# Performance work log

Measured on AMD Instinct MI355X. Metric: run time of the kernel, lower is better.

Reference implementation:

```python
import jax, jax.numpy as jnp
import numpy as np

D = 640          # feature dim (x_dim)
C = 64           # number of classes
N = 1024         # support samples (16 shots/class)
Q = 2048         # query samples
REG = 0.3        # reg_param


def setup_inputs() -> dict:
    key = jax.random.key(0)
    k0, k1, k2, k3, k4 = jax.random.split(key, 5)
    X = jax.random.normal(k0, (N, D), jnp.float32)
    y = (jnp.arange(N) % C).astype(jnp.int32)          # every class populated
    Xq = jax.random.normal(k1, (Q, D), jnp.float32)
    # learnable prior parameters (perturbed from the torch init so grads are nontrivial)
    m = 0.02 * jax.random.normal(k2, (1, D), jnp.float32)
    kappa = jnp.array([0.1], jnp.float32)
    nu = jnp.array([float(D)], jnp.float32)
    triu_diag = 1.0 + 0.05 * jax.random.normal(k3, (D,), jnp.float32)
    triu_lower = jnp.eye(D, dtype=jnp.float32) + 0.05 * jax.random.normal(k4, (D, D), jnp.float32)
    return {"X": X, "y": y, "Xq": Xq, "m": m, "kappa": kappa, "nu": nu,
            "triu_diag": triu_diag, "triu_lower": triu_lower}


def reference(X, y, Xq, m, kappa, nu, triu_diag, triu_lower):
    # strictly-lower-triangular mask: triu(ones, 1).T
    mask = jnp.triu(jnp.ones((D, D), X.dtype), 1).T
    L = jnp.diag(jnp.abs(triu_diag)) + triu_lower * mask          # Cholesky-like factor
    kappa_ = jnp.abs(kappa[0]) + 1e-6
    nu_ = jnp.maximum(nu[0], D - 1 + 1e-6)

    onehot = jax.nn.one_hot(y, C, dtype=X.dtype)                   # [N, C]
    Nc = onehot.sum(0)                                             # [C]
    mean_c = (onehot.T @ X) / Nc[:, None]                          # [C, D]
    # MAP posterior mean per class
    w = Nc / (kappa_ + Nc)
    mu = (1.0 - w)[:, None] * m + w[:, None] * mean_c              # [C, D]

    # per-class second moment: S_c = sum_{y=c} x x^T (segmented X^T X)
    Xc = onehot.T[:, :, None] * X[None, :, :]                      # [C, N, D]
    S = jnp.einsum('cnd,ne->cde', Xc, X)                           # [C, D, D]

    LLt = L @ L.T
    mm = m.T @ m                                                   # [D, D]
    mu_outer = jnp.einsum('cd,ce->cde', mu, mu)
    sigma = (LLt[None] + S + kappa_ * mm[None]
             - (kappa_ + Nc)[:, None, None] * mu_outer)
    sigma = sigma / (nu_ + Nc + D + 2)[:, None, None]
    sigma_inv = jnp.linalg.inv(sigma)
    sigma_inv = (1.0 - REG) * sigma_inv + REG * jnp.eye(D, dtype=X.dtype)

    # batched Mahalanobis quadratic form: -(x - mu_c)^T Sinv_c (x - mu_c)
    diff = Xq[:, None, :] - mu[None, :, :]                         # [Q, C, D]
    dist = jnp.einsum('qcd,cde,qce->qc', diff, sigma_inv, diff)
    return -dist
```

## Files before the change

kernel.cpp:

```cpp
#include <hip/hip_runtime.h>
#include <hip/hip_bf16.h>


#define D 640
#define C 64
#define NSUP 1024
#define Q 2048
#define KMAX 16
#define R18 18
#define VROWS (C * R18)
#define YROWS 3137
#define YPAD 3200
#define NEXT 704

typedef __attribute__((ext_vector_type(8))) short bf16x8;
typedef __attribute__((ext_vector_type(4))) float floatx4;

__device__ __forceinline__ unsigned short f2bf(float x) {
    unsigned int u = __float_as_uint(x);
    unsigned int r = u + 0x7FFFu + ((u >> 16) & 1u);
    return (unsigned short)(r >> 16);
}

__global__ void k_setup(const int* __restrict__ y, const float* __restrict__ kappa,
                        const float* __restrict__ nu, const float* __restrict__ diag,
                        int* __restrict__ cnt, int* __restrict__ idx,
                        float* __restrict__ sc, float* __restrict__ rd,
                        int* __restrict__ rowmap) {
    __shared__ int lc[C];
    int tid = threadIdx.x;
    if (tid < C) lc[tid] = 0;
    __syncthreads();
    for (int n = tid; n < NSUP; n += 256) {
        int c = y[n];
        int k = atomicAdd(&lc[c], 1);
        if (k < KMAX) idx[c * KMAX + k] = n;
    }
    __syncthreads();
    for (int d = tid; d < D; d += 256) rd[d] = 1.0f / fabsf(diag[d]);
    if (tid < C) {
        int n = lc[tid]; if (n > KMAX) n = KMAX;
        cnt[tid] = n;
        float kap = fabsf(kappa[0]) + 1e-6f;
        float nuv = fmaxf(nu[0], (float)(D - 1) + 1e-6f);
        float Ncf = (float)n;
        sc[64 + tid]  = Ncf / (kap + Ncf);
        sc[128 + tid] = nuv + Ncf + (float)(D + 2);
        sc[192 + tid] = -1.0f / (kap + Ncf);
        if (tid == 0) { sc[0] = kap; sc[1] = nuv; }
    }
    __syncthreads();
    for (int i = tid; i < VROWS; i += 256) {
        int c = i / R18, j = i - c * R18;
        int nc = lc[c] < KMAX ? lc[c] : KMAX;
        int rm;
        if (j == 0) rm = Q + NSUP;
        else if (j <= KMAX) rm = (j - 1 < nc) ? Q + idx[c * KMAX + j - 1] : -1;
        else rm = Q + NSUP + 1 + c;
        rowmap[i] = rm;
    }
}

__global__ __launch_bounds__(256) void k_dinv_mu(
        const float* __restrict__ tlow, const float* __restrict__ rd,
        float* __restrict__ Linv,
        const float* __restrict__ X, const float* __restrict__ m,
        const int* __restrict__ cnt, const int* __restrict__ idx,
        const float* __restrict__ sc, float* __restrict__ mu) {
    __shared__ float Lst[128 * 128];
    int tid = threadIdx.x;
    if (blockIdx.x < 160) {
        int bid = blockIdx.x;
        int b = bid >> 5;
        int j = ((bid & 31) << 2) + (tid >> 6);
        int lane = tid & 63;
        int bB = b * 128;
        {
            float4 tv[16];
            float rv[16];
#pragma unroll
            for (int u = 0; u < 16; ++u) {
                int e = tid + u * 256;
                int c4 = (e & 31) * 4, r = e >> 5;
                tv[u] = *(const float4*)(tlow + (size_t)(bB + r) * D + bB + c4);
                rv[u] = rd[bB + r];
            }
#pragma unroll
            for (int u = 0; u < 16; ++u) {
                int e = tid + u * 256;
                int c4 = (e & 31) * 4, r = e >> 5;
                float vv[4] = {tv[u].x, tv[u].y, tv[u].z, tv[u].w};
#pragma unroll
                for (int t = 0; t < 4; ++t) {
                    int c = c4 + t;
                    float v;
                    if (r == c) v = 1.0f;
                    else if (r > c) v = rv[u] * vv[t];
                    else v = 0.f;
                    Lst[c * 128 + (r ^ (c & 63))] = v;
                }
            }
        }
        __syncthreads();
        float rd0 = rd[bB + lane], rd1 = rd[bB + 64 + lane];
        float acc0 = 0.f, acc1 = 0.f, zz0 = 0.f, zz1 = 0.f;
        for (int i = j; i < 128; ++i) {
            int ri = i >> 6, il = i & 63;
            float av = (ri == 0) ? acc0 : acc1;
            float ai = __shfl(av, il);
            float zi = (i == j) ? __shfl((ri == 0) ? rd0 : rd1, il) : -ai;
            int sw = i & 63;
            float l0 = Lst[i * 128 + (lane ^ sw)];
            float l1 = Lst[i * 128 + 64 + (lane ^ sw)];
            if (lane > i) acc0 += l0 * zi;
            if (64 + lane > i) acc1 += l1 * zi;
            if (lane == i) zz0 = zi;
            if (64 + lane == i) zz1 = zi;
        }
        Linv[(size_t)(bB + lane) * D + bB + j] = zz0;
        Linv[(size_t)(bB + 64 + lane) * D + bB + j] = zz1;
    } else {
        int u = (blockIdx.x - 160) * 2 + (tid >> 7);
        int c = u / 5, by = u - c * 5;
        int d = by * 128 + (tid & 127);
        int n = cnt[c];
        float s = 0.f;
        for (int k = 0; k < n; ++k) s += X[(size_t)idx[c * KMAX + k] * D + d];
        float w = sc[64 + c];
        float mean = (n > 0) ? s / (float)n : 0.f;
        mu[(size_t)c * D + d] = (1.f - w) * m[d] + w * mean;
    }
}

__global__ void k_lhat(const float* __restrict__ tlow, const float* __restrict__ Linv,
                       float* __restrict__ Lhat) {
    const int bi_tab[10] = {1, 2, 2, 3, 3, 3, 4, 4, 4, 4};
    const int bk_tab[10] = {0, 0, 1, 0, 1, 2, 0, 1, 2, 3};
    int p = blockIdx.y;
    int bi = bi_tab[p], bk = bk_tab[p];
    int tid = threadIdx.x;
    int c = tid & 127;
    int r = (blockIdx.x << 1) + (tid >> 7);
    const float* drow = Linv + (size_t)(bi * 128 + r) * D + bi * 128;
    const float* lcol = tlow + (size_t)(bi * 128) * D + bk * 128 + c;
    float s = 0.f;
#pragma unroll 4
    for (int t = 0; t < 128; ++t) s += drow[t] * lcol[(size_t)t * D];
    Lhat[(size_t)(bi * 128 + r) * D + bk * 128 + c] = s;
}

template<int B>
__device__ __forceinline__ void linv_chain(const float* __restrict__ Lhat,
                                           float* __restrict__ Linv,
                                           float S[4][128][20],
                                           int cB, int tid) {
    const int ty = tid >> 2, tx = tid & 3;
    const int r0 = 2 * ty;
    float acc[4 - B][2][4];
#pragma unroll
    for (int a = 0; a < 4 - B; ++a)
#pragma unroll
        for (int rr = 0; rr < 2; ++rr)
#pragma unroll
            for (int cc = 0; cc < 4; ++cc) acc[a][rr][cc] = 0.f;
#pragma unroll
    for (int js = 0; js < 4 - B; ++js) {
        const int j = B + js;
        for (int k0 = 0; k0 < 128; k0 += 8) {
            float svf[8][4];
#pragma unroll
            for (int u = 0; u < 8; ++u) {
                float4 s4 = *(const float4*)&S[js][k0 + u][tx * 4];
                svf[u][0] = s4.x; svf[u][1] = s4.y; svf[u][2] = s4.z; svf[u][3] = s4.w;
            }
#pragma unroll
            for (int a = js; a < 4 - B; ++a) {
                const int i = B + 1 + a;
                const float* p0 = Lhat + (size_t)(i * 128 + r0) * D + j * 128 + k0;
                const float* p1 = p0 + D;
                float4 a00 = *(const float4*)(p0);
                float4 a01 = *(const float4*)(p0 + 4);
                float4 a10 = *(const float4*)(p1);
                float4 a11 = *(const float4*)(p1 + 4);
                float ar0[8] = {a00.x, a00.y, a00.z, a00.w, a01.x, a01.y, a01.z, a01.w};
                float ar1[8] = {a10.x, a10.y, a10.z, a10.w, a11.x, a11.y, a11.z, a11.w};
#pragma unroll
                for (int u = 0; u < 8; ++u) {
#pragma unroll
                    for (int cc = 0; cc < 4; ++cc) {
                        acc[a][0][cc] += ar0[u] * svf[u][cc];
                        acc[a][1][cc] += ar1[u] * svf[u][cc];
                    }
                }
            }
        }
        {
            const int i = j + 1;
#pragma unroll
            for (int rr = 0; rr < 2; ++rr) {
                const int r = r0 + rr;
                float4 v;
                v.x = -acc[js][rr][0]; v.y = -acc[js][rr][1];
                v.z = -acc[js][rr][2]; v.w = -acc[js][rr][3];
                if (js + 1 < 4 - B) *(float4*)&S[js + 1][r][tx * 4] = v;
                *(float4*)(Linv + (size_t)(i * 128 + r) * D + cB + tx * 4) = v;
            }
        }
        if (js + 1 < 4 - B) __syncthreads();
    }
}

__global__ __launch_bounds__(256) void k_linv_fill(const float* __restrict__ Lhat,
                                                   float* __restrict__ Linv) {
    __shared__ __align__(16) float S[4][128][20];
    int tid = threadIdx.x;
    int b = blockIdx.x >> 3, strip = blockIdx.x & 7;
    int bB = b * 128, cB = bB + strip * 16;
    {
        int r = tid >> 1, c0 = (tid & 1) * 8;
        const float* src = Linv + (size_t)(bB + r) * D + cB + c0;
        *(float4*)&S[0][r][c0]     = *(const float4*)(src);
        *(float4*)&S[0][r][c0 + 4] = *(const float4*)(src + 4);
    }
    __syncthreads();
    if (b == 0)      linv_chain<0>(Lhat, Linv, S, cB, tid);
    else if (b == 1) linv_chain<1>(Lhat, Linv, S, cB, tid);
    else if (b == 2) linv_chain<2>(Lhat, Linv, S, cB, tid);
    else             linv_chain<3>(Lhat, Linv, S, cB, tid);
}

__device__ __forceinline__ void pack4(const float* vv, unsigned short* hp, unsigned short* lp) {
#pragma unroll
    for (int i = 0; i < 4; ++i) {
        unsigned short hb = f2bf(vv[i]);
        float hf = __uint_as_float((unsigned int)hb << 16);
        hp[i] = hb;
        lp[i] = f2bf(vv[i] - hf);
    }
}

__device__ __forceinline__ void rownorm_body(const float* __restrict__ A, int ld,
                                             float* __restrict__ out, int gw, int lane) {
    const float* row = A + (size_t)gw * ld;
    float s = 0.f;
    for (int d = lane; d < D; d += 64) { float v = row[d]; s += v * v; }
#pragma unroll
    for (int off = 32; off; off >>= 1) s += __shfl_xor(s, off);
    if (lane == 0) out[gw] = s;
}

__global__ void k_packA(const float* __restrict__ Xq, const float* __restrict__ X,
                        const float* __restrict__ m, const float* __restrict__ mu,
                        unsigned short* __restrict__ Ah, unsigned short* __restrict__ Al,
                        const float* __restrict__ Linv,
                        unsigned short* __restrict__ Bh, unsigned short* __restrict__ Bl,
                        float* __restrict__ a0) {
    int bid = blockIdx.x, tid = threadIdx.x;
    if (bid < 2000) {
        int gid = bid * 256 + tid;
        int row = gid / 160, c = (gid - row * 160) * 4;
        if (row >= YPAD) return;
        float4 v = {0.f, 0.f, 0.f, 0.f};
        if (row < Q) v = *(const float4*)(Xq + (size_t)row * D + c);
        else if (row < Q + NSUP) v = *(const float4*)(X + (size_t)(row - Q) * D + c);
        else if (row == Q + NSUP) v = *(const float4*)(m + c);
        else if (row < YROWS) v = *(const float4*)(mu + (size_t)(row - (Q + NSUP + 1)) * D + c);
        float vv[4] = {v.x, v.y, v.z, v.w};
        ushort4 h, l;
        pack4(vv, (unsigned short*)&h, (unsigned short*)&l);
        *(ushort4*)(Ah + (size_t)row * D + c) = h;
        *(ushort4*)(Al + (size_t)row * D + c) = l;
    } else if (bid < 2440) {
        int gid = (bid - 2000) * 256 + tid;
        int row = gid / 160, c = (gid - row * 160) * 4;
        if (row >= NEXT) return;
        float4 v;
        if (row < D) v = *(const float4*)(Linv + (size_t)row * D + c);
        else v = *(const float4*)(mu + (size_t)(row - D) * D + c);
        float vv[4] = {v.x, v.y, v.z, v.w};
#pragma unroll
        for (int i = 0; i < 4; ++i)
            if (row < D && c + i > row) vv[i] = 0.f;
        ushort4 h, l;
        pack4(vv, (unsigned short*)&h, (unsigned short*)&l);
        *(ushort4*)(Bh + (size_t)row * D + c) = h;
        *(ushort4*)(Bl + (size_t)row * D + c) = l;
    } else {
        int gw = ((bid - 2440) * 256 + tid) >> 6;
        rownorm_body(Xq, D, a0, gw, tid & 63);
    }
}

__global__ __launch_bounds__(256) void k_mfma_nt(
        const unsigned short* __restrict__ Ah, const unsigned short* __restrict__ Al,
        const unsigned short* __restrict__ Bh, const unsigned short* __restrict__ Bl,
        const int* __restrict__ rowmap, float* __restrict__ Out,
        int M, int N, int ldo) {
    __shared__ unsigned short Ah_s[64 * 32], Al_s[64 * 32];
    __shared__ unsigned short Bh_s[64 * 32], Bl_s[64 * 32];
    int tid = threadIdx.x;
    int rowBase = blockIdx.y * 64, colBase = blockIdx.x * 64;
    int r = tid >> 2, e = (tid & 3) << 3;
    int gr = rowBase + r;
    int gc = colBase + r;
    int br = (gc < N) ? (rowmap ? rowmap[gc] : gc) : -1;
    bool aok = (gr < M);
    int w = tid >> 6, lane = tid & 63, q = lane >> 4, lr = lane & 15;
    int aoff = (16 * w + lr) * 32 + q * 8;
    const uint4 z4 = {0u, 0u, 0u, 0u};
    floatx4 acc[4] = {{0.f, 0.f, 0.f, 0.f}, {0.f, 0.f, 0.f, 0.f},
                      {0.f, 0.f, 0.f, 0.f}, {0.f, 0.f, 0.f, 0.f}};
    for (int kk = 0; kk < D; kk += 32) {
        uint4 vah = aok ? *(const uint4*)(Ah + (size_t)gr * D + kk + e) : z4;
        uint4 val = aok ? *(const uint4*)(Al + (size_t)gr * D + kk + e) : z4;
        uint4 vbh = (br >= 0) ? *(const uint4*)(Bh + (size_t)br * D + kk + e) : z4;
        uint4 vbl = (br >= 0) ? *(const uint4*)(Bl + (size_t)br * D + kk + e) : z4;
        __syncthreads();
        *(uint4*)(Ah_s + r * 32 + e) = vah;
        *(uint4*)(Al_s + r * 32 + e) = val;
        *(uint4*)(Bh_s + r * 32 + e) = vbh;
        *(uint4*)(Bl_s + r * 32 + e) = vbl;
        __syncthreads();
        bf16x8 ah = *(const bf16x8*)(Ah_s + aoff);
        bf16x8 al = *(const bf16x8*)(Al_s + aoff);
#pragma unroll
        for (int tt = 0; tt < 4; ++tt) {
            int boff = (16 * tt + lr) * 32 + q * 8;
            bf16x8 bh = *(const bf16x8*)(Bh_s + boff);
            bf16x8 bl = *(const bf16x8*)(Bl_s + boff);
            acc[tt] = __builtin_amdgcn_mfma_f32_16x16x32_bf16(ah, bh, acc[tt], 0, 0, 0);
            acc[tt] = __builtin_amdgcn_mfma_f32_16x16x32_bf16(ah, bl, acc[tt], 0, 0, 0);
            acc[tt] = __builtin_amdgcn_mfma_f32_16x16x32_bf16(al, bh, acc[tt], 0, 0, 0);
        }
    }
#pragma unroll
    for (int tt = 0; tt < 4; ++tt) {
        int gc2 = colBase + 16 * tt + lr;
#pragma unroll
        for (int rg = 0; rg < 4; ++rg) {
            int gr2 = rowBase + 16 * w + q * 4 + rg;
            if (gr2 < M && gc2 < N) Out[(size_t)gr2 * ldo + gc2] = acc[tt][rg];
        }
    }
}

__global__ __launch_bounds__(256) void k_packB(
        const float* __restrict__ Yt, const int* __restrict__ rowmap,
        const float* __restrict__ mu, const float* __restrict__ sc,
        unsigned short* __restrict__ Th, unsigned short* __restrict__ Tl,
        float* __restrict__ at,
        float* __restrict__ h, float* __restrict__ btil,
        float* __restrict__ b0, float* __restrict__ kinv) {
    __shared__ __align__(16) float sv[R18][644];
    __shared__ float aug[R18][40];
    __shared__ int rmv[R18];
    int tid = threadIdx.x;
    if (blockIdx.x < 64) {
        int c = blockIdx.x;
        if (tid < R18) rmv[tid] = rowmap[c * R18 + tid];
        __syncthreads();
        {
            int rmu[12];
#pragma unroll
            for (int u = 0; u < 12; ++u) {
                int i = tid + u * 256;
                int r = i / 160;
                rmu[u] = (i < R18 * 160) ? rmv[r] : -1;
            }
            float4 buf[12];
            const float4 z = {0.f, 0.f, 0.f, 0.f};
#pragma unroll
            for (int u = 0; u < 12; ++u) {
                int i = tid + u * 256;
                int d4 = (i - (i / 160) * 160) * 4;
                buf[u] = (rmu[u] >= 0) ? *(const float4*)(Yt + (size_t)rmu[u] * NEXT + d4) : z;
            }
#pragma unroll
            for (int u = 0; u < 12; ++u) {
                int i = tid + u * 256;
                if (i < R18 * 160) {
                    int r = i / 160, d4 = (i - r * 160) * 4;
                    *(float4*)&sv[r][d4] = buf[u];
                }
            }
        }
        __syncthreads();
        if (tid < 171) {
            int i = 0, rem = tid;
            while (rem >= R18 - i) { rem -= R18 - i; ++i; }
            int j = i + rem;
            const float* ri = sv[i];
            const float* rj = sv[j];
            float s0 = 0.f, s1 = 0.f, s2 = 0.f, s3 = 0.f;
#pragma unroll 4
            for (int d = 0; d < D; d += 4) {
                float4 a = *(const float4*)(ri + d);
                float4 bb = *(const float4*)(rj + d);
                s0 += a.x * bb.x; s1 += a.y * bb.y;
                s2 += a.z * bb.z; s3 += a.w * bb.w;
            }
            float s = (s0 + s1) + (s2 + s3);
            aug[i][j] = s;
            if (i != j) aug[j][i] = s;
        }
        for (int i2 = tid; i2 < R18 * R18; i2 += 256)
            aug[i2 / R18][R18 + i2 % R18] = (i2 / R18 == i2 % R18) ? 1.f : 0.f;
        __syncthreads();
        int w = tid >> 6, lane = tid & 63;
        if (w == 1) {
            const float* mc = mu + (size_t)c * D;
            float s = 0.f;
            for (int d = lane; d < D; d += 64) { float v = mc[d]; s += v * v; }
#pragma unroll
            for (int off = 32; off; off >>= 1) s += __shfl_xor(s, off);
            if (lane == 0) b0[c] = s;
        }
        if (w == 0) {
            if (lane < R18) h[c * R18 + lane] = aug[lane][R18 - 1];
            if (lane == 0) btil[c] = aug[R18 - 1][R18 - 1];
            volatile float (*va)[40] = (volatile float (*)[40])aug;
            if (lane == 0) va[0][0] += 1.0f / sc[0];
            else if (lane <= KMAX) va[lane][lane] += 1.0f;
            else if (lane == R18 - 1) va[R18 - 1][R18 - 1] += sc[192 + c];
            __threadfence_block();
            for (int p = 0; p < R18; ++p) {
                float v = (lane >= p && lane < R18) ? fabsf(va[lane][p]) : -1.f;
                int bi = lane;
#pragma unroll
                for (int off = 32; off; off >>= 1) {
                    float ov = __shfl_xor(v, off);
                    int oi = __shfl_xor(bi, off);
                    if (ov > v || (ov == v && oi < bi)) { v = ov; bi = oi; }
                }
                float pv = va[bi][p];
                if (lane < 2 * R18) {
                    float rp = va[bi][lane];
                    if (bi != p) va[bi][lane] = va[p][lane];
                    va[p][lane] = rp / pv;
                }
                __threadfence_block();
                float f  = (lane < R18) ? va[lane][p] : 0.f;
                float pr = (lane < 2 * R18) ? va[p][lane] : 0.f;
#pragma unroll
                for (int it = 0; it < 11; ++it) {
                    int e = lane + it * 64;
                    int r2 = e / 36, cc = e - r2 * 36;
                    float fr = __shfl(f, r2 < R18 ? r2 : 0);
                    float pc = __shfl(pr, cc);
                    if (e < R18 * 2 * R18 && r2 != p) va[r2][cc] -= fr * pc;
                }
                __threadfence_block();
            }
            for (int e = lane; e < R18 * R18; e += 64)
                kinv[(size_t)c * R18 * R18 + e] = va[e / R18][R18 + e % R18];
        }
    } else if (blockIdx.x < 2064) {
        int gid = (blockIdx.x - 64) * 256 + tid;
        int row = gid / 160, c = (gid - row * 160) * 4;
        if (row >= YPAD) return;
        float4 v = *(const float4*)(Yt + (size_t)row * NEXT + c);
        float vv[4] = {v.x, v.y, v.z, v.w};
        ushort4 hh, ll;
        pack4(vv, (unsigned short*)&hh, (unsigned short*)&ll);
        *(ushort4*)(Th + (size_t)row * D + c) = hh;
        *(ushort4*)(Tl + (size_t)row * D + c) = ll;
    } else {
        int gw = ((blockIdx.x - 2064) * 256 + tid) >> 6;
        rownorm_body(Yt, NEXT, at, gw, tid & 63);
    }
}

__global__ void k_epi(const float* __restrict__ G, const float* __restrict__ Yt,
                      const float* __restrict__ at, const float* __restrict__ a0,
                      const float* __restrict__ h, const float* __restrict__ btil,
                      const float* __restrict__ b0, const float* __restrict__ kinv,
                      const float* __restrict__ sc, float* __restrict__ out) {
    __shared__ float lk[R18 * R18], lh[R18];
    __shared__ float ldn, lbt, lb0;
    int c = blockIdx.x, tid = threadIdx.x;
    for (int i = tid; i < R18 * R18; i += 256) lk[i] = kinv[(size_t)c * R18 * R18 + i];
    if (tid < R18) lh[tid] = h[c * R18 + tid];
    if (tid == 0) { ldn = sc[128 + c]; lbt = btil[c]; lb0 = b0[c]; }
    __syncthreads();
    int q = blockIdx.y * 256 + tid;
    const float* Gr = G + (size_t)q * VROWS + c * R18;
    float g[R18];
#pragma unroll
    for (int j = 0; j < R18; ++j) g[j] = Gr[j];
    float ipt = g[R18 - 1];
#pragma unroll
    for (int j = 0; j < R18; ++j) g[j] -= lh[j];
    float corr = 0.f;
#pragma unroll
    for (int i = 0; i < R18; ++i) {
        float s = 0.f;
#pragma unroll
        for (int j = 0; j < R18; ++j) s += lk[i * R18 + j] * g[j];
        corr += g[i] * s;
    }
    float ip0 = Yt[(size_t)q * NEXT + D + c];
    float tt = at[q] - 2.f * ipt + lbt;
    float t0 = a0[q] - 2.f * ip0 + lb0;
    out[(size_t)q * C + c] = -(0.7f * ldn * (tt - corr) + 0.3f * t0);
}

extern "C" void kernel_launch(void* const* d_in, const int* in_sizes, int n_in,
                              void* d_out, int out_size, void* d_ws, size_t ws_size,
                              hipStream_t stream) {
    const float* X     = (const float*)d_in[0];
    const int*   y     = (const int*)d_in[1];
    const float* Xq    = (const float*)d_in[2];
    const float* m     = (const float*)d_in[3];
    const float* kappa = (const float*)d_in[4];
    const float* nu    = (const float*)d_in[5];
    const float* tdiag = (const float*)d_in[6];
    const float* tlow  = (const float*)d_in[7];
    float* out = (float*)d_out;

    char* w = (char*)d_ws;
    auto alloc = [&](size_t bytes) {
        char* p = w;
        w += (bytes + 255) & ~(size_t)255;
        return p;
    };
    int*   cnt    = (int*)alloc(C * 4);
    int*   idx    = (int*)alloc(C * KMAX * 4);
    int*   rowmap = (int*)alloc(VROWS * 4);
    float* sc     = (float*)alloc(256 * 4);
    float* rd     = (float*)alloc(D * 4);
    float* mu     = (float*)alloc((size_t)C * D * 4);
    float* at     = (float*)alloc(Q * 4);
    float* a0     = (float*)alloc(Q * 4);
    float* h      = (float*)alloc(C * R18 * 4);
    float* btil   = (float*)alloc(C * 4);
    float* b0     = (float*)alloc(C * 4);
    float* kinv   = (float*)alloc((size_t)C * R18 * R18 * 4);
    float* Ytout  = (float*)alloc((size_t)YPAD * NEXT * 4);
    unsigned short* Th = (unsigned short*)alloc((size_t)YPAD * D * 2);
    unsigned short* Tl = (unsigned short*)alloc((size_t)YPAD * D * 2);
    unsigned short* Bh = (unsigned short*)alloc((size_t)NEXT * D * 2);
    unsigned short* Bl = (unsigned short*)alloc((size_t)NEXT * D * 2);
    char* wmark = w;
    float* Linv = (float*)alloc((size_t)D * D * 4);
    float* Lhat = (float*)alloc((size_t)D * D * 4);
    unsigned short* Ah = (unsigned short*)alloc((size_t)YPAD * D * 2);
    unsigned short* Al = (unsigned short*)alloc((size_t)YPAD * D * 2);
    w = wmark;
    float* G    = (float*)alloc((size_t)Q * VROWS * 4);

    k_setup<<<1, 256, 0, stream>>>(y, kappa, nu, tdiag, cnt, idx, sc, rd, rowmap);
    k_dinv_mu<<<320, 256, 0, stream>>>(tlow, rd, Linv, X, m, cnt, idx, sc, mu);
    k_lhat<<<dim3(64, 10), 256, 0, stream>>>(tlow, Linv, Lhat);
    k_linv_fill<<<32, 256, 0, stream>>>(Lhat, Linv);
    k_packA<<<2952, 256, 0, stream>>>(Xq, X, m, mu, Ah, Al, Linv, Bh, Bl, a0);
    k_mfma_nt<<<dim3(NEXT / 64, YPAD / 64), 256, 0, stream>>>(
        Ah, Al, Bh, Bl, nullptr, Ytout, YPAD, NEXT, NEXT);
    k_packB<<<2576, 256, 0, stream>>>(Ytout, rowmap, mu, sc, Th, Tl, at, h, btil, b0, kinv);
    k_mfma_nt<<<dim3(VROWS / 64, Q / 64), 256, 0, stream>>>(
        Th, Tl, Th, Tl, rowmap, G, Q, VROWS, VROWS);
    k_epi<<<dim3(C, Q / 256), 256, 0, stream>>>(G, Ytout, at, a0, h, btil, b0, kinv, sc, out);
}
```

Baseline: 243.8 us.

## Fuse bf16 split packing into producer kernels and merge GEMM with packB

Removes the standalone k_packA and k_packB passes. The bf16 hi/lo split of Linv, mu, Xq, X and m is now produced directly in k_dinv_mu, k_linv_fill and k_setup, with k_setup also zero-filling the padding. The first GEMM's epilogue writes the Th/Tl split of its output. The second GEMM is folded into a combined k_gv kernel alongside the per-class kinv and row-norm work. This cuts two launches and one full read/write pass over the Yt intermediate, at the cost of more scattered 2-byte stores and larger, more heterogeneous kernels.

New measurement: 219.1 us. -10.1%, faster.

```diff
diff --git a/kernel.cpp b/kernel.cpp
--- a/kernel.cpp
+++ b/kernel.cpp
@@ -22,13 +22,46 @@
     return (unsigned short)(r >> 16);
 }
 
+__device__ __forceinline__ void pack4(const float* vv, unsigned short* hp, unsigned short* lp) {
+#pragma unroll
+    for (int i = 0; i < 4; ++i) {
+        unsigned short hb = f2bf(vv[i]);
+        float hf = __uint_as_float((unsigned int)hb << 16);
+        hp[i] = hb;
+        lp[i] = f2bf(vv[i] - hf);
+    }
+}
+
+__device__ __forceinline__ void rownorm_body(const float* __restrict__ A, int ld,
+                                             float* __restrict__ out, int gw, int lane) {
+    const float* row = A + (size_t)gw * ld;
+    float s = 0.f;
+    for (int d = lane; d < D; d += 64) { float v = row[d]; s += v * v; }
+#pragma unroll
+    for (int off = 32; off; off >>= 1) s += __shfl_xor(s, off);
+    if (lane == 0) out[gw] = s;
+}
+
+#define BZCH (640 * 640 / 8)
+#define AZCH (63 * 640 / 8)
 __global__ void k_setup(const int* __restrict__ y, const float* __restrict__ kappa,
                         const float* __restrict__ nu, const float* __restrict__ diag,
                         int* __restrict__ cnt, int* __restrict__ idx,
                         float* __restrict__ sc, float* __restrict__ rd,
-                        int* __restrict__ rowmap) {
+                        int* __restrict__ rowmap,
+                        unsigned short* __restrict__ Ah, unsigned short* __restrict__ Al,
+                        unsigned short* __restrict__ Bh, unsigned short* __restrict__ Bl) {
+    int tid = threadIdx.x;
+    if (blockIdx.x > 0) {
+        int id = (blockIdx.x - 1) * 256 + tid;
+        const uint4 z = {0u, 0u, 0u, 0u};
+        if (id < BZCH) ((uint4*)Bh)[id] = z;
+        else if (id < 2 * BZCH) ((uint4*)Bl)[id - BZCH] = z;
+        else if (id < 2 * BZCH + AZCH) ((uint4*)(Ah + (size_t)YROWS * D))[id - 2 * BZCH] = z;
+        else if (id < 2 * BZCH + 2 * AZCH) ((uint4*)(Al + (size_t)YROWS * D))[id - 2 * BZCH - AZCH] = z;
+        return;
+    }
     __shared__ int lc[C];
-    int tid = threadIdx.x;
     if (tid < C) lc[tid] = 0;
     __syncthreads();
     for (int n = tid; n < NSUP; n += 256) {
@@ -66,11 +99,15 @@
         float* __restrict__ Linv,
         const float* __restrict__ X, const float* __restrict__ m,
         const int* __restrict__ cnt, const int* __restrict__ idx,
-        const float* __restrict__ sc, float* __restrict__ mu) {
+        const float* __restrict__ sc, float* __restrict__ mu,
+        const float* __restrict__ Xq,
+        unsigned short* __restrict__ Ah, unsigned short* __restrict__ Al,
+        unsigned short* __restrict__ Bh, unsigned short* __restrict__ Bl,
+        float* __restrict__ a0) {
     __shared__ float Lst[128 * 128];
     int tid = threadIdx.x;
-    if (blockIdx.x < 160) {
-        int bid = blockIdx.x;
+    int bid = blockIdx.x;
+    if (bid < 160) {
         int b = bid >> 5;
         int j = ((bid & 31) << 2) + (tid >> 6);
         int lane = tid & 63;
@@ -119,8 +156,16 @@
         }
         Linv[(size_t)(bB + lane) * D + bB + j] = zz0;
         Linv[(size_t)(bB + 64 + lane) * D + bB + j] = zz1;
-    } else {
-        int u = (blockIdx.x - 160) * 2 + (tid >> 7);
+        unsigned short h0 = f2bf(zz0);
+        float hf0 = __uint_as_float((unsigned int)h0 << 16);
+        Bh[(size_t)(bB + lane) * D + bB + j] = h0;
+        Bl[(size_t)(bB + lane) * D + bB + j] = f2bf(zz0 - hf0);
+        unsigned short h1 = f2bf(zz1);
+        float hf1 = __uint_as_float((unsigned int)h1 << 16);
+        Bh[(size_t)(bB + 64 + lane) * D + bB + j] = h1;
+        Bl[(size_t)(bB + 64 + lane) * D + bB + j] = f2bf(zz1 - hf1);
+    } else if (bid < 320) {
+        int u = (bid - 160) * 2 + (tid >> 7);
         int c = u / 5, by = u - c * 5;
         int d = by * 128 + (tid & 127);
         int n = cnt[c];
@@ -128,7 +173,38 @@
         for (int k = 0; k < n; ++k) s += X[(size_t)idx[c * KMAX + k] * D + d];
         float w = sc[64 + c];
         float mean = (n > 0) ? s / (float)n : 0.f;
-        mu[(size_t)c * D + d] = (1.f - w) * m[d] + w * mean;
+        float val = (1.f - w) * m[d] + w * mean;
+        mu[(size_t)c * D + d] = val;
+        unsigned short hb = f2bf(val);
+        float hf = __uint_as_float((unsigned int)hb << 16);
+        unsigned short lb = f2bf(val - hf);
+        Ah[(size_t)(Q + NSUP + 1 + c) * D + d] = hb;
+        Al[(size_t)(Q + NSUP + 1 + c) * D + d] = lb;
+        Bh[(size_t)(D + c) * D + d] = hb;
+        Bl[(size_t)(D + c) * D + d] = lb;
+    } else if (bid < 2240) {
+        int gid = (bid - 320) * 256 + tid;
+        int row = gid / 160, c = (gid - row * 160) * 4;
+        float4 v = (row < Q) ? *(const float4*)(Xq + (size_t)row * D + c)
+                             : *(const float4*)(X + (size_t)(row - Q) * D + c);
+        float vv[4] = {v.x, v.y, v.z, v.w};
+        ushort4 h, l;
+        pack4(vv, (unsigned short*)&h, (unsigned short*)&l);
+        *(ushort4*)(Ah + (size_t)row * D + c) = h;
+        *(ushort4*)(Al + (size_t)row * D + c) = l;
+    } else if (bid == 2240) {
+        if (tid < 160) {
+            int c = tid * 4;
+            float4 v = *(const float4*)(m + c);
+            float vv[4] = {v.x, v.y, v.z, v.w};
+            ushort4 h, l;
+            pack4(vv, (unsigned short*)&h, (unsigned short*)&l);
+            *(ushort4*)(Ah + (size_t)(Q + NSUP) * D + c) = h;
+            *(ushort4*)(Al + (size_t)(Q + NSUP) * D + c) = l;
+        }
+    } else {
+        int gw = ((bid - 2241) * 256 + tid) >> 6;
+        rownorm_body(Xq, D, a0, gw, tid & 63);
     }
 }
 
@@ -152,6 +228,8 @@
 template<int B>
 __device__ __forceinline__ void linv_chain(const float* __restrict__ Lhat,
                                            float* __restrict__ Linv,
+                                           unsigned short* __restrict__ Bh,
+                                           unsigned short* __restrict__ Bl,
                                            float S[4][128][20],
                                            int cB, int tid) {
     const int ty = tid >> 2, tx = tid & 3;
@@ -199,11 +277,16 @@
 #pragma unroll
             for (int rr = 0; rr < 2; ++rr) {
                 const int r = r0 + rr;
-                float4 v;
-                v.x = -acc[js][rr][0]; v.y = -acc[js][rr][1];
-                v.z = -acc[js][rr][2]; v.w = -acc[js][rr][3];
+                float vv[4];
+#pragma unroll
+                for (int cc = 0; cc < 4; ++cc) vv[cc] = -acc[js][rr][cc];
+                float4 v = {vv[0], vv[1], vv[2], vv[3]};
                 if (js + 1 < 4 - B) *(float4*)&S[js + 1][r][tx * 4] = v;
                 *(float4*)(Linv + (size_t)(i * 128 + r) * D + cB + tx * 4) = v;
+                ushort4 hh, ll;
+                pack4(vv, (unsigned short*)&hh, (unsigned short*)&ll);
+                *(ushort4*)(Bh + (size_t)(i * 128 + r) * D + cB + tx * 4) = hh;
+                *(ushort4*)(Bl + (size_t)(i * 128 + r) * D + cB + tx * 4) = ll;
             }
         }
         if (js + 1 < 4 - B) __syncthreads();
@@ -211,7 +294,9 @@
 }
 
 __global__ __launch_bounds__(256) void k_linv_fill(const float* __restrict__ Lhat,
-                                                   float* __restrict__ Linv) {
+                                                   float* __restrict__ Linv,
+                                                   unsigned short* __restrict__ Bh,
+                                                   unsigned short* __restrict__ Bl) {
     __shared__ __align__(16) float S[4][128][20];
     int tid = threadIdx.x;
     int b = blockIdx.x >> 3, strip = blockIdx.x & 7;
@@ -223,79 +308,17 @@
         *(float4*)&S[0][r][c0 + 4] = *(const float4*)(src + 4);
     }
     __syncthreads();
-    if (b == 0)      linv_chain<0>(Lhat, Linv, S, cB, tid);
-    else if (b == 1) linv_chain<1>(Lhat, Linv, S, cB, tid);
-    else if (b == 2) linv_chain<2>(Lhat, Linv, S, cB, tid);
-    else             linv_chain<3>(Lhat, Linv, S, cB, tid);
-}
-
-__device__ __forceinline__ void pack4(const float* vv, unsigned short* hp, unsigned short* lp) {
-#pragma unroll
-    for (int i = 0; i < 4; ++i) {
-        unsigned short hb = f2bf(vv[i]);
-        float hf = __uint_as_float((unsigned int)hb << 16);
-        hp[i] = hb;
-        lp[i] = f2bf(vv[i] - hf);
-    }
-}
-
-__device__ __forceinline__ void rownorm_body(const float* __restrict__ A, int ld,
-                                             float* __restrict__ out, int gw, int lane) {
-    const float* row = A + (size_t)gw * ld;
-    float s = 0.f;
-    for (int d = lane; d < D; d += 64) { float v = row[d]; s += v * v; }
-#pragma unroll
-    for (int off = 32; off; off >>= 1) s += __shfl_xor(s, off);
-    if (lane == 0) out[gw] = s;
-}
-
-__global__ void k_packA(const float* __restrict__ Xq, const float* __restrict__ X,
-                        const float* __restrict__ m, const float* __restrict__ mu,
-                        unsigned short* __restrict__ Ah, unsigned short* __restrict__ Al,
-                        const float* __restrict__ Linv,
-                        unsigned short* __restrict__ Bh, unsigned short* __restrict__ Bl,
-                        float* __restrict__ a0) {
-    int bid = blockIdx.x, tid = threadIdx.x;
-    if (bid < 2000) {
-        int gid = bid * 256 + tid;
-        int row = gid / 160, c = (gid - row * 160) * 4;
-        if (row >= YPAD) return;
-        float4 v = {0.f, 0.f, 0.f, 0.f};
-        if (row < Q) v = *(const float4*)(Xq + (size_t)row * D + c);
-        else if (row < Q + NSUP) v = *(const float4*)(X + (size_t)(row - Q) * D + c);
-        else if (row == Q + NSUP) v = *(const float4*)(m + c);
-        else if (row < YROWS) v = *(const float4*)(mu + (size_t)(row - (Q + NSUP + 1)) * D + c);
-        float vv[4] = {v.x, v.y, v.z, v.w};
-        ushort4 h, l;
-        pack4(vv, (unsigned short*)&h, (unsigned short*)&l);
-        *(ushort4*)(Ah + (size_t)row * D + c) = h;
-        *(ushort4*)(Al + (size_t)row * D + c) = l;
-    } else if (bid < 2440) {
-        int gid = (bid - 2000) * 256 + tid;
-        int row = gid / 160, c = (gid - row * 160) * 4;
-        if (row >= NEXT) return;
-        float4 v;
-        if (row < D) v = *(const float4*)(Linv + (size_t)row * D + c);
-        else v = *(const float4*)(mu + (size_t)(row - D) * D + c);
-        float vv[4] = {v.x, v.y, v.z, v.w};
-#pragma unroll
-        for (int i = 0; i < 4; ++i)
-            if (row < D && c + i > row) vv[i] = 0.f;
-        ushort4 h, l;
-        pack4(vv, (unsigned short*)&h, (unsigned short*)&l);
-        *(ushort4*)(Bh + (size_t)row * D + c) = h;
-        *(ushort4*)(Bl + (size_t)row * D + c) = l;
-    } else {
-        int gw = ((bid - 2440) * 256 + tid) >> 6;
-        rownorm_body(Xq, D, a0, gw, tid & 63);
-    }
+    if (b == 0)      linv_chain<0>(Lhat, Linv, Bh, Bl, S, cB, tid);
+    else if (b == 1) linv_chain<1>(Lhat, Linv, Bh, Bl, S, cB, tid);
+    else if (b == 2) linv_chain<2>(Lhat, Linv, Bh, Bl, S, cB, tid);
+    else             linv_chain<3>(Lhat, Linv, Bh, Bl, S, cB, tid);
 }
 
 __global__ __launch_bounds__(256) void k_mfma_nt(
         const unsigned short* __restrict__ Ah, const unsigned short* __restrict__ Al,
         const unsigned short* __restrict__ Bh, const unsigned short* __restrict__ Bl,
-        const int* __restrict__ rowmap, float* __restrict__ Out,
-        int M, int N, int ldo) {
+        float* __restrict__ Out, int M, int N, int ldo,
+        unsigned short* __restrict__ Th, unsigned short* __restrict__ Tl) {
     __shared__ unsigned short Ah_s[64 * 32], Al_s[64 * 32];
     __shared__ unsigned short Bh_s[64 * 32], Bl_s[64 * 32];
     int tid = threadIdx.x;
@@ -303,8 +326,7 @@
     int r = tid >> 2, e = (tid & 3) << 3;
     int gr = rowBase + r;
     int gc = colBase + r;
-    int br = (gc < N) ? (rowmap ? rowmap[gc] : gc) : -1;
-    bool aok = (gr < M);
+    bool aok = (gr < M), bok = (gc < N);
     int w = tid >> 6, lane = tid & 63, q = lane >> 4, lr = lane & 15;
     int aoff = (16 * w + lr) * 32 + q * 8;
     const uint4 z4 = {0u, 0u, 0u, 0u};
@@ -313,8 +335,8 @@
     for (int kk = 0; kk < D; kk += 32) {
         uint4 vah = aok ? *(const uint4*)(Ah + (size_t)gr * D + kk + e) : z4;
         uint4 val = aok ? *(const uint4*)(Al + (size_t)gr * D + kk + e) : z4;
-        uint4 vbh = (br >= 0) ? *(const uint4*)(Bh + (size_t)br * D + kk + e) : z4;
-        uint4 vbl = (br >= 0) ? *(const uint4*)(Bl + (size_t)br * D + kk + e) : z4;
+        uint4 vbh = bok ? *(const uint4*)(Bh + (size_t)gc * D + kk + e) : z4;
+        uint4 vbl = bok ? *(const uint4*)(Bl + (size_t)gc * D + kk + e) : z4;
         __syncthreads();
         *(uint4*)(Ah_s + r * 32 + e) = vah;
         *(uint4*)(Al_s + r * 32 + e) = val;
@@ -339,24 +361,34 @@
 #pragma unroll
         for (int rg = 0; rg < 4; ++rg) {
             int gr2 = rowBase + 16 * w + q * 4 + rg;
-            if (gr2 < M && gc2 < N) Out[(size_t)gr2 * ldo + gc2] = acc[tt][rg];
-        }
-    }
-}
-
-__global__ __launch_bounds__(256) void k_packB(
-        const float* __restrict__ Yt, const int* __restrict__ rowmap,
-        const float* __restrict__ mu, const float* __restrict__ sc,
-        unsigned short* __restrict__ Th, unsigned short* __restrict__ Tl,
-        float* __restrict__ at,
+            if (gr2 < M && gc2 < N) {
+                float v = acc[tt][rg];
+                Out[(size_t)gr2 * ldo + gc2] = v;
+                if (Th && gc2 < D) {
+                    unsigned short hb = f2bf(v);
+                    float hf = __uint_as_float((unsigned int)hb << 16);
+                    Th[(size_t)gr2 * D + gc2] = hb;
+                    Tl[(size_t)gr2 * D + gc2] = f2bf(v - hf);
+                }
+            }
+        }
+    }
+}
+
+__global__ __launch_bounds__(256) void k_gv(
+        const unsigned short* __restrict__ Th, const unsigned short* __restrict__ Tl,
+        const int* __restrict__ rowmap, float* __restrict__ G,
+        const float* __restrict__ Yt, const float* __restrict__ mu,
+        const float* __restrict__ sc, float* __restrict__ at,
         float* __restrict__ h, float* __restrict__ btil,
         float* __restrict__ b0, float* __restrict__ kinv) {
-    __shared__ __align__(16) float sv[R18][644];
-    __shared__ float aug[R18][40];
-    __shared__ int rmv[R18];
-    int tid = threadIdx.x;
-    if (blockIdx.x < 64) {
-        int c = blockIdx.x;
+    __shared__ __align__(16) char smem[49344];
+    int bid = blockIdx.x, tid = threadIdx.x;
+    if (bid < 64) {
+        float (*sv)[644] = (float(*)[644])smem;
+        float (*aug)[40] = (float(*)[40])(smem + 46368);
+        int* rmv = (int*)(smem + 46368 + 2880);
+        int c = bid;
         if (tid < R18) rmv[tid] = rowmap[c * R18 + tid];
         __syncthreads();
         {
@@ -454,18 +486,56 @@
             for (int e = lane; e < R18 * R18; e += 64)
                 kinv[(size_t)c * R18 * R18 + e] = va[e / R18][R18 + e % R18];
         }
-    } else if (blockIdx.x < 2064) {
-        int gid = (blockIdx.x - 64) * 256 + tid;
-        int row = gid / 160, c = (gid - row * 160) * 4;
-        if (row >= YPAD) return;
-        float4 v = *(const float4*)(Yt + (size_t)row * NEXT + c);
-        float vv[4] = {v.x, v.y, v.z, v.w};
-        ushort4 hh, ll;
-        pack4(vv, (unsigned short*)&hh, (unsigned short*)&ll);
-        *(ushort4*)(Th + (size_t)row * D + c) = hh;
-        *(ushort4*)(Tl + (size_t)row * D + c) = ll;
+    } else if (bid < 640) {
+        unsigned short* Ah_s = (unsigned short*)smem;
+        unsigned short* Al_s = (unsigned short*)(smem + 4096);
+        unsigned short* Bh_s = (unsigned short*)(smem + 8192);
+        unsigned short* Bl_s = (unsigned short*)(smem + 12288);
+        int gb = bid - 64;
+        int rowBase = (gb / 18) * 64, colBase = (gb % 18) * 64;
+        int r = tid >> 2, e = (tid & 3) << 3;
+        int gr = rowBase + r;
+        int gc = colBase + r;
+        int br = rowmap[gc];
+        int w = tid >> 6, lane = tid & 63, q = lane >> 4, lr = lane & 15;
+        int aoff = (16 * w + lr) * 32 + q * 8;
+        const uint4 z4 = {0u, 0u, 0u, 0u};
+        floatx4 acc[4] = {{0.f, 0.f, 0.f, 0.f}, {0.f, 0.f, 0.f, 0.f},
+                          {0.f, 0.f, 0.f, 0.f}, {0.f, 0.f, 0.f, 0.f}};
+        for (int kk = 0; kk < D; kk += 32) {
+            uint4 vah = *(const uint4*)(Th + (size_t)gr * D + kk + e);
+            uint4 val = *(const uint4*)(Tl + (size_t)gr * D + kk + e);
+            uint4 vbh = (br >= 0) ? *(const uint4*)(Th + (size_t)br * D + kk + e) : z4;
+            uint4 vbl = (br >= 0) ? *(const uint4*)(Tl + (size_t)br * D + kk + e) : z4;
+            __syncthreads();
+            *(uint4*)(Ah_s + r * 32 + e) = vah;
+            *(uint4*)(Al_s + r * 32 + e) = val;
+            *(uint4*)(Bh_s + r * 32 + e) = vbh;
+            *(uint4*)(Bl_s + r * 32 + e) = vbl;
+            __syncthreads();
+            bf16x8 ah = *(const bf16x8*)(Ah_s + aoff);
+            bf16x8 al = *(const bf16x8*)(Al_s + aoff);
+#pragma unroll
+            for (int tt = 0; tt < 4; ++tt) {
+                int boff = (16 * tt + lr) * 32 + q * 8;
+                bf16x8 bh = *(const bf16x8*)(Bh_s + boff);
+                bf16x8 bl = *(const bf16x8*)(Bl_s + boff);
+                acc[tt] = __builtin_amdgcn_mfma_f32_16x16x32_bf16(ah, bh, acc[tt], 0, 0, 0);
+                acc[tt] = __builtin_amdgcn_mfma_f32_16x16x32_bf16(ah, bl, acc[tt], 0, 0, 0);
+                acc[tt] = __builtin_amdgcn_mfma_f32_16x16x32_bf16(al, bh, acc[tt], 0, 0, 0);
+            }
+        }
+#pragma unroll
+        for (int tt = 0; tt < 4; ++tt) {
+            int gc2 = colBase + 16 * tt + lr;
+#pragma unroll
+            for (int rg = 0; rg < 4; ++rg) {
+                int gr2 = rowBase + 16 * w + q * 4 + rg;
+                G[(size_t)gr2 * VROWS + gc2] = acc[tt][rg];
+            }
+        }
     } else {
-        int gw = ((blockIdx.x - 2064) * 256 + tid) >> 6;
+        int gw = ((bid - 640) * 256 + tid) >> 6;
         rownorm_body(Yt, NEXT, at, gw, tid & 63);
     }
 }
@@ -548,15 +618,15 @@
     w = wmark;
     float* G    = (float*)alloc((size_t)Q * VROWS * 4);
 
-    k_setup<<<1, 256, 0, stream>>>(y, kappa, nu, tdiag, cnt, idx, sc, rd, rowmap);
-    k_dinv_mu<<<320, 256, 0, stream>>>(tlow, rd, Linv, X, m, cnt, idx, sc, mu);
+    k_setup<<<441, 256, 0, stream>>>(y, kappa, nu, tdiag, cnt, idx, sc, rd, rowmap,
+                                     Ah, Al, Bh, Bl);
+    k_dinv_mu<<<2753, 256, 0, stream>>>(tlow, rd, Linv, X, m, cnt, idx, sc, mu,
+                                        Xq, Ah, Al, Bh, Bl, a0);
     k_lhat<<<dim3(64, 10), 256, 0, stream>>>(tlow, Linv, Lhat);
-    k_linv_fill<<<32, 256, 0, stream>>>(Lhat, Linv);
-    k_packA<<<2952, 256, 0, stream>>>(Xq, X, m, mu, Ah, Al, Linv, Bh, Bl, a0);
+    k_linv_fill<<<32, 256, 0, stream>>>(Lhat, Linv, Bh, Bl);
     k_mfma_nt<<<dim3(NEXT / 64, YPAD / 64), 256, 0, stream>>>(
-        Ah, Al, Bh, Bl, nullptr, Ytout, YPAD, NEXT, NEXT);
-    k_packB<<<2576, 256, 0, stream>>>(Ytout, rowmap, mu, sc, Th, Tl, at, h, btil, b0, kinv);
-    k_mfma_nt<<<dim3(VROWS / 64, Q / 64), 256, 0, stream>>>(
-        Th, Tl, Th, Tl, rowmap, G, Q, VROWS, VROWS);
+        Ah, Al, Bh, Bl, Ytout, YPAD, NEXT, NEXT, Th, Tl);
+    k_gv<<<1152, 256, 0, stream>>>(Th, Tl, rowmap, G, Ytout, mu, sc, at,
+                                   h, btil, b0, kinv);
     k_epi<<<dim3(C, Q / 256), 256, 0, stream>>>(G, Ytout, at, a0, h, btil, b0, kinv, sc, out);
 }
```
